# Optimization experiments

Hardware: AMD Instinct MI355X
Metric: run time of the kernel (lower is better)

The kernel has to match this reference:

```python
import jax, jax.numpy as jnp
import numpy as np

NUM_TABLES = 26
VOCAB = 100000
D = 128          # sparse_feature_size == mlp_bot[-1]
B = 8192
P = 10           # fixed pooling factor per bag
DENSE = 13
BOT = [512, 256, 128]
TOP = [1024, 1024, 512, 256, 1]
NF = NUM_TABLES + 1  # features entering dot interaction


def setup_inputs() -> dict:
    key = jax.random.key(0)
    ks = iter(jax.random.split(key, 32))
    inp = {}
    inp["dense_x"] = jax.random.normal(next(ks), (B, DENSE), dtype=jnp.float32)
    inp["sparse_indices"] = jax.random.randint(next(ks), (NUM_TABLES, B * P), 0, VOCAB, dtype=jnp.int32)
    # EmbeddingBag weights init: uniform(-0.01, 0.01)
    inp["emb_tables"] = jax.random.uniform(next(ks), (NUM_TABLES, VOCAB, D), jnp.float32, -0.01, 0.01)
    def xavier(k, shape):
        fan_out, fan_in = shape
        lim = np.sqrt(6.0 / (fan_in + fan_out)).astype(np.float32)
        return jax.random.uniform(k, shape, jnp.float32, -lim, lim)
    dims_bot = [DENSE] + BOT
    for i in range(len(BOT)):
        inp[f"bot_w{i}"] = xavier(next(ks), (dims_bot[i + 1], dims_bot[i]))
        inp[f"bot_b{i}"] = jnp.zeros((dims_bot[i + 1],), jnp.float32)
    interact_dim = NF * (NF - 1) // 2 + BOT[-1]  # 351 + 128 = 479
    dims_top = [interact_dim] + TOP
    for i in range(len(TOP)):
        inp[f"top_w{i}"] = xavier(next(ks), (dims_top[i + 1], dims_top[i]))
        inp[f"top_b{i}"] = jnp.zeros((dims_top[i + 1],), jnp.float32)
    return inp


def reference(dense_x, sparse_indices, emb_tables,
              bot_w0, bot_b0, bot_w1, bot_b1, bot_w2, bot_b2,
              top_w0, top_b0, top_w1, top_b1, top_w2, top_b2,
              top_w3, top_b3, top_w4, top_b4):
    # bottom MLP (Linear + ReLU on every layer)
    x = dense_x
    for w, b in ((bot_w0, bot_b0), (bot_w1, bot_b1), (bot_w2, bot_b2)):
        x = jax.nn.relu(x @ w.T + b)  # [B, 128]

    # multi-table EmbeddingBag sum pooling (fixed pooling factor P)
    idx = sparse_indices.reshape(NUM_TABLES, B, P)
    ly = jax.vmap(lambda tab, i: tab[i].sum(axis=1))(emb_tables, idx)  # [T, B, D]

    # dot interaction: bmm + upper-triangular gather
    T_feat = jnp.concatenate([x[None], ly], axis=0).transpose(1, 0, 2)  # [B, NF, D]
    Z = jnp.einsum('bnd,bmd->bnm', T_feat, T_feat)                       # [B, NF, NF]
    li, lj = np.triu_indices(NF, k=1)
    Zflat = Z[:, li, lj]                                                 # [B, NF*(NF-1)/2]
    z = jnp.concatenate([x, Zflat], axis=1)                              # [B, 479]

    # top MLP: ReLU on all but last layer
    h = z
    tops = ((top_w0, top_b0), (top_w1, top_b1), (top_w2, top_b2), (top_w3, top_b3))
    for w, b in tops:
        h = jax.nn.relu(h @ w.T + b)
    p = h @ top_w4.T + top_b4  # [B, 1]
    return jax.nn.sigmoid(p.squeeze(1))
```

## Files before the change

kernel.cpp:

```cpp
#include <hip/hip_runtime.h>
#include <hip/hip_bf16.h>
#include <cstdint>

typedef __attribute__((ext_vector_type(8))) short bf16x8;
typedef __attribute__((ext_vector_type(4))) short bf16x4;
typedef __attribute__((ext_vector_type(4))) float f32x4;

#define B_SZ 8192
#define TROW 3456

__device__ __forceinline__ void gld_lds16(const void* g, void* l) {
    __builtin_amdgcn_global_load_lds(
        (const __attribute__((address_space(1))) unsigned int*)g,
        (__attribute__((address_space(3))) unsigned int*)l, 16, 0, 0);
}

__device__ __forceinline__ short f2bf_bits(float v) {
    return __builtin_bit_cast(short, __float2bfloat16(v));
}

struct CvtJob { const float* in; __hip_bfloat16* out; int N, K, Kp; };
struct CvtJobs { CvtJob j[6]; int start[7]; };

__device__ __forceinline__ void cvt_dev8(int lb, int tid, const CvtJobs& J) {
    int chunk = lb * 256 + tid;
    int e = chunk * 8;
    if (e >= J.start[6]) return;
    int k = 0;
    #pragma unroll
    for (int i = 1; i < 6; i++) if (e >= J.start[i]) k = i;
    const CvtJob& job = J.j[k];
    int local = e - J.start[k];
    float v[8];
    if (job.K == job.Kp) {
        const float4* p = (const float4*)(job.in + local);
        float4 a = p[0], b = p[1];
        v[0]=a.x; v[1]=a.y; v[2]=a.z; v[3]=a.w; v[4]=b.x; v[5]=b.y; v[6]=b.z; v[7]=b.w;
    } else {
        int n = local / job.Kp, kk = local - n * job.Kp;
        #pragma unroll
        for (int i = 0; i < 8; i++)
            v[i] = (kk + i < job.K) ? job.in[(size_t)n * job.K + kk + i] : 0.f;
    }
    bf16x8 o;
    #pragma unroll
    for (int i = 0; i < 8; i++)
        o[i] = f2bf_bits(v[i]);
    *(bf16x8*)(job.out + local) = o;
}

__device__ __forceinline__ void bot0_dev(int lb, int tid, const float* __restrict__ x,
    const float* __restrict__ w, const float* __restrict__ bias,
    __hip_bfloat16* __restrict__ o, float* xs) {
    int m0 = lb * 4;
    if (tid < 52) xs[tid] = x[(size_t)m0 * 13 + tid];
    __syncthreads();
    for (int c = tid; c < 512; c += 256) {
        const float* wr = w + (size_t)c * 13;
        float bv = bias[c];
        #pragma unroll
        for (int r = 0; r < 4; r++) {
            float s = bv;
            #pragma unroll
            for (int k = 0; k < 13; k++) s += xs[r * 13 + k] * wr[k];
            o[(size_t)(m0 + r) * 512 + c] = __float2bfloat16(fmaxf(s, 0.f));
        }
    }
}

__device__ __forceinline__ void emb_dev(int lb, int tid, int t0,
    const int* __restrict__ idx, const float* __restrict__ tab,
    __hip_bfloat16* __restrict__ T) {
    int lane = tid & 63, wv = tid >> 6;
    int p = lb * 4 + wv;
    int t = t0 + (p >> 13);
    int b = p & 8191;
    const int* ip = idx + (size_t)t * 81920 + b * 10;
    const float* tb = tab + (size_t)t * 100000 * 128;
    int half = lane >> 5, l32 = lane & 31;
    float4 s = {0.f, 0.f, 0.f, 0.f};
    #pragma unroll
    for (int j = 0; j < 10; j += 2) {
        int r = ip[j + half];
        float4 v = ((const float4*)(tb + (size_t)r * 128))[l32];
        s.x += v.x; s.y += v.y; s.z += v.z; s.w += v.w;
    }
    s.x += __shfl_xor(s.x, 32, 64);
    s.y += __shfl_xor(s.y, 32, 64);
    s.z += __shfl_xor(s.z, 32, 64);
    s.w += __shfl_xor(s.w, 32, 64);
    if (half == 0) {
        bf16x4 o;
        o[0] = f2bf_bits(s.x); o[1] = f2bf_bits(s.y);
        o[2] = f2bf_bits(s.z); o[3] = f2bf_bits(s.w);
        ((bf16x4*)(T + (size_t)b * TROW + (1 + t) * 128))[l32] = o;
    }
}

template<int TM, int TN, int WM, int WN>
__device__ __forceinline__ void gemm_dev(int tileId, int nTiles, int nbx, int tid,
    const __hip_bfloat16* __restrict__ A, const __hip_bfloat16* __restrict__ W,
    const float* __restrict__ bias, __hip_bfloat16* __restrict__ C,
    int K, int ldc, __hip_bfloat16* ABs) {
    constexpr int ROWS = TM + TN;
    constexpr int CH = ROWS * 4 / 256;
    constexpr int MI = TM / WM / 16;
    constexpr int NI = TN / WN / 16;

    int swz = tileId;
    if ((nTiles & 7) == 0) {
        int q = nTiles >> 3;
        swz = (tileId & 7) * q + (tileId >> 3);
    }
    const int by = swz / nbx, bx = swz - by * nbx;
    const int m0 = by * TM, n0 = bx * TN;

    const int lane = tid & 63, wave = tid >> 6;
    const int wmI = wave / WN, wnI = wave % WN;

    const __hip_bfloat16* gp[CH];
    #pragma unroll
    for (int c = 0; c < CH; c++) {
        int gid = c * 256 + tid;
        int row = gid >> 2, col = (gid & 3) * 8;
        gp[c] = (row < TM ? A + (size_t)(m0 + row) * K
                          : W + (size_t)(n0 + row - TM) * K) + col;
    }

    f32x4 acc[MI][NI] = {};
    const int fr = lane & 15, fkb = (lane >> 4) * 8;

    for (int k0 = 0; k0 < K; k0 += 32) {
        __syncthreads();
        #pragma unroll
        for (int c = 0; c < CH; c++)
            gld_lds16(gp[c] + k0, &ABs[(c * 256 + wave * 64) * 8]);
        asm volatile("s_waitcnt vmcnt(0)" ::: "memory");
        __syncthreads();
        bf16x8 a[MI], b[NI];
        #pragma unroll
        for (int i = 0; i < MI; i++)
            a[i] = *(const bf16x8*)&ABs[(wmI * (TM / WM) + i * 16 + fr) * 32 + fkb];
        #pragma unroll
        for (int j = 0; j < NI; j++)
            b[j] = *(const bf16x8*)&ABs[(TM + wnI * (TN / WN) + j * 16 + fr) * 32 + fkb];
        #pragma unroll
        for (int i = 0; i < MI; i++)
            #pragma unroll
            for (int j = 0; j < NI; j++)
                acc[i][j] = __builtin_amdgcn_mfma_f32_16x16x32_bf16(a[i], b[j], acc[i][j], 0, 0, 0);
    }

    const int fq = lane >> 4;
    #pragma unroll
    for (int i = 0; i < MI; i++) {
        #pragma unroll
        for (int j = 0; j < NI; j++) {
            int n = n0 + wnI * (TN / WN) + j * 16 + fr;
            float bv = bias[n];
            #pragma unroll
            for (int r = 0; r < 4; r++) {
                int m = m0 + wmI * (TM / WM) + i * 16 + fq * 4 + r;
                C[(size_t)m * ldc + n] = __float2bfloat16(fmaxf(acc[i][j][r] + bv, 0.f));
            }
        }
    }
}

template<int TM, int TN, int WM, int WN>
__global__ __launch_bounds__(256) void gemm_k(const __hip_bfloat16* A, const __hip_bfloat16* W,
                                              const float* bias, __hip_bfloat16* C,
                                              int nbx, int K, int ldc) {
    __shared__ __align__(16) __hip_bfloat16 ABs[(TM + TN) * 32];
    gemm_dev<TM, TN, WM, WN>(blockIdx.x, gridDim.x, nbx, threadIdx.x, A, W, bias, C, K, ldc, ABs);
}

__global__ __launch_bounds__(256) void k_pre_emb(CvtJobs J, int cvtB,
    const float* dx, const float* w0, const float* b0, __hip_bfloat16* bufA,
    int t0, const int* sidx, const float* tab, __hip_bfloat16* T) {
    __shared__ float xs[64];
    int blk = blockIdx.x, tid = threadIdx.x;
    if (blk < cvtB) { cvt_dev8(blk, tid, J); return; }
    blk -= cvtB;
    if (blk < B_SZ / 4) { bot0_dev(blk, tid, dx, w0, b0, bufA, xs); return; }
    emb_dev(blk - B_SZ / 4, tid, t0, sidx, tab, T);
}

__global__ __launch_bounds__(256) void k_gemm_emb(const __hip_bfloat16* A, const __hip_bfloat16* W,
    const float* bias, __hip_bfloat16* C, int nbx, int K, int ldc, int gB,
    int t0, const int* sidx, const float* tab, __hip_bfloat16* T) {
    __shared__ __align__(16) __hip_bfloat16 ABs[(128 + 64) * 32];
    if (blockIdx.x < gB)
        gemm_dev<128, 64, 2, 2>(blockIdx.x, gB, nbx, threadIdx.x, A, W, bias, C, K, ldc, ABs);
    else
        emb_dev(blockIdx.x - gB, threadIdx.x, t0, sidx, tab, T);
}

__global__ __launch_bounds__(256) void k_int(const __hip_bfloat16* __restrict__ T,
                                             __hip_bfloat16* __restrict__ z) {
    int lane = threadIdx.x & 63, wave = threadIdx.x >> 6;
    int b = blockIdx.x * 4 + wave;
    const __hip_bfloat16* Tb = T + (size_t)b * TROW;

    const int fr = lane & 15, fkb = (lane >> 4) * 8;
    bf16x8 fr2[2][4];
    #pragma unroll
    for (int mi = 0; mi < 2; mi++)
        #pragma unroll
        for (int kt = 0; kt < 4; kt++)
            fr2[mi][kt] = *(const bf16x8*)&Tb[(mi * 16 + fr) * 128 + kt * 32 + fkb];

    f32x4 acc[2][2] = {};
    #pragma unroll
    for (int kt = 0; kt < 4; kt++)
        #pragma unroll
        for (int mi = 0; mi < 2; mi++)
            #pragma unroll
            for (int ni = 0; ni < 2; ni++)
                acc[mi][ni] = __builtin_amdgcn_mfma_f32_16x16x32_bf16(fr2[mi][kt], fr2[ni][kt], acc[mi][ni], 0, 0, 0);

    __hip_bfloat16* zb = z + (size_t)b * 512;
    ((unsigned*)zb)[lane] = ((const unsigned*)Tb)[lane];
    if (lane < 33) zb[479 + lane] = __float2bfloat16(0.f);
    const int fq = lane >> 4;
    #pragma unroll
    for (int mi = 0; mi < 2; mi++)
        #pragma unroll
        for (int ni = 0; ni < 2; ni++)
            #pragma unroll
            for (int r = 0; r < 4; r++) {
                int m = mi * 16 + fq * 4 + r;
                int n = ni * 16 + fr;
                if (m < 27 && n < 27 && m < n) {
                    int p = m * 26 - (m * (m - 1)) / 2 + (n - m - 1);
                    zb[128 + p] = __float2bfloat16(acc[mi][ni][r]);
                }
            }
}

__global__ __launch_bounds__(256) void final_kernel(const __hip_bfloat16* __restrict__ h,
                                                    const float* __restrict__ w,
                                                    const float* __restrict__ bias,
                                                    float* __restrict__ out) {
    int lane = threadIdx.x & 63, wv = threadIdx.x >> 6;
    int s = blockIdx.x * 4 + wv;
    const __hip_bfloat16* hp = h + (size_t)s * 256;
    float sum = 0.f;
    #pragma unroll
    for (int i = 0; i < 4; i++) {
        int k = i * 64 + lane;
        sum += __bfloat162float(hp[k]) * w[k];
    }
    #pragma unroll
    for (int off = 32; off; off >>= 1) sum += __shfl_down(sum, off, 64);
    if (lane == 0) out[s] = 1.f / (1.f + expf(-(sum + bias[0])));
}

extern "C" void kernel_launch(void* const* d_in, const int* in_sizes, int n_in,
                              void* d_out, int out_size, void* d_ws, size_t ws_size,
                              hipStream_t stream) {
    const float* dense_x = (const float*)d_in[0];
    const int* sidx      = (const int*)d_in[1];
    const float* emb     = (const float*)d_in[2];
    const float* bw0 = (const float*)d_in[3];  const float* bb0 = (const float*)d_in[4];
    const float* bw1 = (const float*)d_in[5];  const float* bb1 = (const float*)d_in[6];
    const float* bw2 = (const float*)d_in[7];  const float* bb2 = (const float*)d_in[8];
    const float* tw0 = (const float*)d_in[9];  const float* tb0 = (const float*)d_in[10];
    const float* tw1 = (const float*)d_in[11]; const float* tb1 = (const float*)d_in[12];
    const float* tw2 = (const float*)d_in[13]; const float* tb2 = (const float*)d_in[14];
    const float* tw3 = (const float*)d_in[15]; const float* tb3 = (const float*)d_in[16];
    const float* tw4 = (const float*)d_in[17]; const float* tb4 = (const float*)d_in[18];
    float* out = (float*)d_out;

    char* ws = (char*)d_ws;
    size_t off = 0;
    auto alloc = [&](size_t bytes) {
        off = (off + 255) & ~(size_t)255;
        void* p = ws + off;
        off += bytes;
        return p;
    };
    __hip_bfloat16* Wb1 = (__hip_bfloat16*)alloc((size_t)256 * 512 * 2);
    __hip_bfloat16* Wb2 = (__hip_bfloat16*)alloc((size_t)128 * 256 * 2);
    __hip_bfloat16* Wt0 = (__hip_bfloat16*)alloc((size_t)1024 * 512 * 2);
    __hip_bfloat16* Wt1 = (__hip_bfloat16*)alloc((size_t)1024 * 1024 * 2);
    __hip_bfloat16* Wt2 = (__hip_bfloat16*)alloc((size_t)512 * 1024 * 2);
    __hip_bfloat16* Wt3 = (__hip_bfloat16*)alloc((size_t)256 * 512 * 2);
    __hip_bfloat16* bufA = (__hip_bfloat16*)alloc((size_t)B_SZ * 512 * 2);
    __hip_bfloat16* bufB = (__hip_bfloat16*)alloc((size_t)B_SZ * 256 * 2);
    __hip_bfloat16* Tbuf = (__hip_bfloat16*)alloc((size_t)B_SZ * TROW * 2);
    __hip_bfloat16* zbuf = (__hip_bfloat16*)alloc((size_t)B_SZ * 512 * 2);
    __hip_bfloat16* h0   = (__hip_bfloat16*)alloc((size_t)B_SZ * 1024 * 2);
    __hip_bfloat16* h1   = (__hip_bfloat16*)alloc((size_t)B_SZ * 1024 * 2);
    __hip_bfloat16* h2   = (__hip_bfloat16*)alloc((size_t)B_SZ * 512 * 2);
    __hip_bfloat16* h3   = (__hip_bfloat16*)alloc((size_t)B_SZ * 256 * 2);

    CvtJobs J;
    auto setJob = [&](int i, const float* in, __hip_bfloat16* o, int N, int K, int Kp) {
        J.j[i] = {in, o, N, K, Kp};
    };
    setJob(0, bw1, Wb1, 256, 512, 512);
    setJob(1, bw2, Wb2, 128, 256, 256);
    setJob(2, tw0, Wt0, 1024, 479, 512);
    setJob(3, tw1, Wt1, 1024, 1024, 1024);
    setJob(4, tw2, Wt2, 512, 1024, 1024);
    setJob(5, tw3, Wt3, 256, 512, 512);
    J.start[0] = 0;
    for (int i = 0; i < 6; i++) J.start[i + 1] = J.start[i] + J.j[i].N * J.j[i].Kp;
    const int cvtB = (J.start[6] / 8 + 255) / 256;

    k_pre_emb<<<cvtB + B_SZ / 4 + 13 * B_SZ / 4, 256, 0, stream>>>(
        J, cvtB, dense_x, bw0, bb0, bufA, 0, sidx, emb, Tbuf);

    k_gemm_emb<<<256 + 13 * B_SZ / 4, 256, 0, stream>>>(
        bufA, Wb1, bb1, bufB, 256 / 64, 512, 256, 256, 13, sidx, emb, Tbuf);

    gemm_k< 64, 64, 2, 2><<<(B_SZ / 64) * (128 / 64), 256, 0, stream>>>(bufB, Wb2, bb2, Tbuf, 128 / 64, 256, TROW);

    k_int<<<B_SZ / 4, 256, 0, stream>>>(Tbuf, zbuf);

    gemm_k<128,128, 2, 2><<<(B_SZ / 128) * (1024 / 128), 256, 0, stream>>>(zbuf, Wt0, tb0, h0, 1024 / 128, 512, 1024);
    gemm_k<128,128, 2, 2><<<(B_SZ / 128) * (1024 / 128), 256, 0, stream>>>(h0, Wt1, tb1, h1, 1024 / 128, 1024, 1024);
    gemm_k<128,128, 2, 2><<<(B_SZ / 128) * ( 512 / 128), 256, 0, stream>>>(h1, Wt2, tb2, h2, 512 / 128, 1024, 512);
    gemm_k<128, 64, 2, 2><<<(B_SZ / 128) * ( 256 /  64), 256, 0, stream>>>(h2, Wt3, tb3, h3, 256 / 64, 512, 256);

    final_kernel<<<B_SZ / 4, 256, 0, stream>>>(h3, tw4, tb4, out);
}
```

Before: 312.2 us.

## Fuse last top-MLP layer with final projection and spread embeddings over bottom GEMMs

Replaces the last top-MLP GEMM plus the separate dot/sigmoid kernel with one kernel. It computes ReLU(h2·W3+b3)·w4 in registers, reduces across lanes and waves, and writes the sigmoid output, so the h3 buffer and its round trip go away. The embedding bag work is also redistributed as 9, 8 and 9 tables across three launches, with the bottom-layer-2 GEMM now co-scheduled with embedding blocks. The fused kernel launches only 128 blocks with a single-buffered K loop, which may underuse the GPU.

New measurement: 307.7 us. No clear change (-1.4%).

```diff
diff --git a/kernel.cpp b/kernel.cpp
--- a/kernel.cpp
+++ b/kernel.cpp
@@ -186,12 +186,13 @@
     emb_dev(blk - B_SZ / 4, tid, t0, sidx, tab, T);
 }
 
+template<int TM, int TN>
 __global__ __launch_bounds__(256) void k_gemm_emb(const __hip_bfloat16* A, const __hip_bfloat16* W,
     const float* bias, __hip_bfloat16* C, int nbx, int K, int ldc, int gB,
     int t0, const int* sidx, const float* tab, __hip_bfloat16* T) {
-    __shared__ __align__(16) __hip_bfloat16 ABs[(128 + 64) * 32];
+    __shared__ __align__(16) __hip_bfloat16 ABs[(TM + TN) * 32];
     if (blockIdx.x < gB)
-        gemm_dev<128, 64, 2, 2>(blockIdx.x, gB, nbx, threadIdx.x, A, W, bias, C, K, ldc, ABs);
+        gemm_dev<TM, TN, 2, 2>(blockIdx.x, gB, nbx, threadIdx.x, A, W, bias, C, K, ldc, ABs);
     else
         emb_dev(blockIdx.x - gB, threadIdx.x, t0, sidx, tab, T);
 }
@@ -238,22 +239,86 @@
             }
 }
 
-__global__ __launch_bounds__(256) void final_kernel(const __hip_bfloat16* __restrict__ h,
-                                                    const float* __restrict__ w,
-                                                    const float* __restrict__ bias,
-                                                    float* __restrict__ out) {
-    int lane = threadIdx.x & 63, wv = threadIdx.x >> 6;
-    int s = blockIdx.x * 4 + wv;
-    const __hip_bfloat16* hp = h + (size_t)s * 256;
-    float sum = 0.f;
-    #pragma unroll
-    for (int i = 0; i < 4; i++) {
-        int k = i * 64 + lane;
-        sum += __bfloat162float(hp[k]) * w[k];
-    }
-    #pragma unroll
-    for (int off = 32; off; off >>= 1) sum += __shfl_down(sum, off, 64);
-    if (lane == 0) out[s] = 1.f / (1.f + expf(-(sum + bias[0])));
+__global__ __launch_bounds__(256) void k_top3_fin(const __hip_bfloat16* __restrict__ A,
+                                                  const __hip_bfloat16* __restrict__ W,
+                                                  const float* __restrict__ b3,
+                                                  const float* __restrict__ w4,
+                                                  const float* __restrict__ b4,
+                                                  float* __restrict__ out) {
+    constexpr int TM = 64, TN = 256, K = 512;
+    constexpr int ROWS = TM + TN;
+    constexpr int CH = ROWS * 4 / 256;
+    __shared__ __align__(16) __hip_bfloat16 ABs[ROWS * 32];
+    __shared__ float red[4 * 64];
+
+    const int tid = threadIdx.x;
+    const int lane = tid & 63, wave = tid >> 6;
+    const int m0 = blockIdx.x * TM;
+
+    const __hip_bfloat16* gp[CH];
+    #pragma unroll
+    for (int c = 0; c < CH; c++) {
+        int gid = c * 256 + tid;
+        int row = gid >> 2, col = (gid & 3) * 8;
+        gp[c] = (row < TM ? A + (size_t)(m0 + row) * K
+                          : W + (size_t)(row - TM) * K) + col;
+    }
+
+    f32x4 acc[4][4] = {};
+    const int fr = lane & 15, fkb = (lane >> 4) * 8;
+
+    for (int k0 = 0; k0 < K; k0 += 32) {
+        __syncthreads();
+        #pragma unroll
+        for (int c = 0; c < CH; c++)
+            gld_lds16(gp[c] + k0, &ABs[(c * 256 + wave * 64) * 8]);
+        asm volatile("s_waitcnt vmcnt(0)" ::: "memory");
+        __syncthreads();
+        bf16x8 a[4], b[4];
+        #pragma unroll
+        for (int i = 0; i < 4; i++)
+            a[i] = *(const bf16x8*)&ABs[(i * 16 + fr) * 32 + fkb];
+        #pragma unroll
+        for (int j = 0; j < 4; j++)
+            b[j] = *(const bf16x8*)&ABs[(TM + wave * 64 + j * 16 + fr) * 32 + fkb];
+        #pragma unroll
+        for (int i = 0; i < 4; i++)
+            #pragma unroll
+            for (int j = 0; j < 4; j++)
+                acc[i][j] = __builtin_amdgcn_mfma_f32_16x16x32_bf16(a[i], b[j], acc[i][j], 0, 0, 0);
+    }
+
+    float p[4][4] = {};
+    #pragma unroll
+    for (int j = 0; j < 4; j++) {
+        int n = wave * 64 + j * 16 + fr;
+        float bv = b3[n], wv = w4[n];
+        #pragma unroll
+        for (int i = 0; i < 4; i++)
+            #pragma unroll
+            for (int r = 0; r < 4; r++)
+                p[i][r] += fmaxf(acc[i][j][r] + bv, 0.f) * wv;
+    }
+    #pragma unroll
+    for (int mask = 1; mask < 16; mask <<= 1)
+        #pragma unroll
+        for (int i = 0; i < 4; i++)
+            #pragma unroll
+            for (int r = 0; r < 4; r++)
+                p[i][r] += __shfl_xor(p[i][r], mask, 64);
+    const int fq = lane >> 4;
+    if (fr == 0) {
+        #pragma unroll
+        for (int i = 0; i < 4; i++)
+            #pragma unroll
+            for (int r = 0; r < 4; r++)
+                red[wave * 64 + i * 16 + fq * 4 + r] = p[i][r];
+    }
+    __syncthreads();
+    if (tid < 64) {
+        float s = red[tid] + red[64 + tid] + red[128 + tid] + red[192 + tid];
+        out[m0 + tid] = 1.f / (1.f + expf(-(s + b4[0])));
+    }
 }
 
 extern "C" void kernel_launch(void* const* d_in, const int* in_sizes, int n_in,
@@ -293,7 +358,6 @@
     __hip_bfloat16* h0   = (__hip_bfloat16*)alloc((size_t)B_SZ * 1024 * 2);
     __hip_bfloat16* h1   = (__hip_bfloat16*)alloc((size_t)B_SZ * 1024 * 2);
     __hip_bfloat16* h2   = (__hip_bfloat16*)alloc((size_t)B_SZ * 512 * 2);
-    __hip_bfloat16* h3   = (__hip_bfloat16*)alloc((size_t)B_SZ * 256 * 2);
 
     CvtJobs J;
     auto setJob = [&](int i, const float* in, __hip_bfloat16* o, int N, int K, int Kp) {
@@ -308,21 +372,22 @@
     J.start[0] = 0;
     for (int i = 0; i < 6; i++) J.start[i + 1] = J.start[i] + J.j[i].N * J.j[i].Kp;
     const int cvtB = (J.start[6] / 8 + 255) / 256;
-
-    k_pre_emb<<<cvtB + B_SZ / 4 + 13 * B_SZ / 4, 256, 0, stream>>>(
+    const int EMB_T = B_SZ / 4;
+
+    k_pre_emb<<<cvtB + B_SZ / 4 + 9 * EMB_T, 256, 0, stream>>>(
         J, cvtB, dense_x, bw0, bb0, bufA, 0, sidx, emb, Tbuf);
 
-    k_gemm_emb<<<256 + 13 * B_SZ / 4, 256, 0, stream>>>(
-        bufA, Wb1, bb1, bufB, 256 / 64, 512, 256, 256, 13, sidx, emb, Tbuf);
-
-    gemm_k< 64, 64, 2, 2><<<(B_SZ / 64) * (128 / 64), 256, 0, stream>>>(bufB, Wb2, bb2, Tbuf, 128 / 64, 256, TROW);
+    k_gemm_emb<128, 64><<<256 + 8 * EMB_T, 256, 0, stream>>>(
+        bufA, Wb1, bb1, bufB, 256 / 64, 512, 256, 256, 9, sidx, emb, Tbuf);
+
+    k_gemm_emb<64, 64><<<256 + 9 * EMB_T, 256, 0, stream>>>(
+        bufB, Wb2, bb2, Tbuf, 128 / 64, 256, TROW, 256, 17, sidx, emb, Tbuf);
 
     k_int<<<B_SZ / 4, 256, 0, stream>>>(Tbuf, zbuf);
 
     gemm_k<128,128, 2, 2><<<(B_SZ / 128) * (1024 / 128), 256, 0, stream>>>(zbuf, Wt0, tb0, h0, 1024 / 128, 512, 1024);
     gemm_k<128,128, 2, 2><<<(B_SZ / 128) * (1024 / 128), 256, 0, stream>>>(h0, Wt1, tb1, h1, 1024 / 128, 1024, 1024);
     gemm_k<128,128, 2, 2><<<(B_SZ / 128) * ( 512 / 128), 256, 0, stream>>>(h1, Wt2, tb2, h2, 512 / 128, 1024, 512);
-    gemm_k<128, 64, 2, 2><<<(B_SZ / 128) * ( 256 /  64), 256, 0, stream>>>(h2, Wt3, tb3, h3, 256 / 64, 512, 256);
-
-    final_kernel<<<B_SZ / 4, 256, 0, stream>>>(h3, tw4, tb4, out);
-}
+
+    k_top3_fin<<<B_SZ / 64, 256, 0, stream>>>(h2, Wt3, tb3, tw4, tb4, out);
+}
```
